# Optimization experiments

Measured on AMD Instinct MI355X. Metric: run time of the kernel, lower is better.

Reference implementation:

```python
import jax, jax.numpy as jnp
import numpy as np

N_BCH = 8        # molecules per batch
N_ATM = 10000    # atoms per molecule
N_EDGE = 5_120_000  # ~avg degree 64
N_ELM = 100      # element-type table size


def setup_inputs() -> dict:
    key = jax.random.key(0)
    k1, k2, k3, k4, k5, k6, k7 = jax.random.split(key, 7)
    elm = jax.random.randint(k1, (N_BCH, N_ATM), 0, N_ELM)
    edge_n = jax.random.randint(k2, (N_EDGE,), 0, N_BCH)
    edge_i = jax.random.randint(k3, (N_EDGE,), 0, N_ATM)
    edge_j = jax.random.randint(k4, (N_EDGE,), 0, N_ATM)
    # squared distances in [0, 4) -> dis in [0, 2)
    sod = jax.random.uniform(k5, (N_EDGE,), dtype=jnp.float32) * 4.0
    # per-element force constant and radius (positive)
    k_param = jax.random.uniform(k6, (N_ELM,), dtype=jnp.float32) + 0.5
    radius = jax.random.uniform(k7, (N_ELM,), dtype=jnp.float32) * 0.5 + 0.5
    return {"elm": elm, "edge_n": edge_n, "edge_i": edge_i, "edge_j": edge_j,
            "sod": sod, "k": k_param, "radius": radius}


def reference(elm, edge_n, edge_i, edge_j, sod, k, radius):
    # gather per-edge element types
    ei = elm[edge_n, edge_i]          # [E]
    ej = elm[edge_n, edge_j]          # [E]
    dis = jnp.sqrt(sod)               # [E]
    kk = k[ei] + k[ej]                # [E]
    R = radius[ei] + radius[ej]       # [E]
    mask = dis < R
    d = dis - R
    eng_bnd = jnp.where(mask, kk * d * d, jnp.zeros((), dtype=sod.dtype))  # [E]
    # scatter-add per atom: flat index n*n_atm + i
    seg = edge_n * N_ATM + edge_i
    eng_atm = jax.ops.segment_sum(eng_bnd, seg, num_segments=N_BCH * N_ATM)
    eng_atm = eng_atm.reshape(N_BCH, N_ATM)
    eng_mol = eng_atm.sum(axis=1)     # [n_bch]
    return eng_mol
```

## Files before the change

kernel.cpp:

```cpp
#include <hip/hip_runtime.h>
#include <hip/hip_bf16.h>
#include <hip/hip_fp16.h>

#define N_BCH 8
#define N_ATM 10000
#define N_ELM 100
#define N_ATOMS_TOT 80000
#define NBLK 256
#define NTHR 1024

typedef int   i4 __attribute__((ext_vector_type(4)));
typedef float f4 __attribute__((ext_vector_type(4)));

__launch_bounds__(1024, 4)
__global__ void edge_kernel(const int* __restrict__ elm,
                            const float* __restrict__ kparam,
                            const float* __restrict__ radius,
                            const int* __restrict__ edge_n,
                            const int* __restrict__ edge_i,
                            const int* __restrict__ edge_j,
                            const float* __restrict__ sod,
                            float* __restrict__ out,
                            int nE) {
    __shared__ unsigned int s_elm32[N_ATOMS_TOT / 4];
    __shared__ __half2 s_kr[128];
    __shared__ float s_red[16][N_BCH];

    for (int t = threadIdx.x; t < N_ATOMS_TOT / 4; t += NTHR) {
        i4 v = *(const i4*)(elm + 4 * t);
        s_elm32[t] = (unsigned int)(v[0] & 0xff)
                   | ((unsigned int)(v[1] & 0xff) << 8)
                   | ((unsigned int)(v[2] & 0xff) << 16)
                   | ((unsigned int)(v[3] & 0xff) << 24);
    }
    if (threadIdx.x < N_ELM)
        s_kr[threadIdx.x] =
            __floats2half2_rn(kparam[threadIdx.x], radius[threadIdx.x]);
    __syncthreads();

    const unsigned char* s_elm = (const unsigned char*)s_elm32;

    float acc[N_BCH];
#pragma unroll
    for (int b = 0; b < N_BCH; ++b) acc[b] = 0.0f;

    const int nvec  = nE >> 2;
    const int chunk = (nvec + NBLK - 1) / NBLK;
    const int base  = blockIdx.x * chunk;
    const int vmax  = min(base + chunk, nvec);
    const int nsweep = (chunk + NTHR - 1) / NTHR;

    const i4* en4 = (const i4*)edge_n;
    const i4* ei4 = (const i4*)edge_i;
    const i4* ej4 = (const i4*)edge_j;
    const f4* s4  = (const f4*)sod;

    int  v  = base + threadIdx.x;
    bool pv = v < vmax;
    int  vc = pv ? v : 0;
    i4 nn = __builtin_nontemporal_load(en4 + vc);
    i4 ii = __builtin_nontemporal_load(ei4 + vc);
    i4 jj = __builtin_nontemporal_load(ej4 + vc);
    f4 ss = __builtin_nontemporal_load(s4  + vc);

    for (int s = 0; s < nsweep; ++s) {
        int  v2  = v + NTHR;
        bool pv2 = v2 < vmax;
        int  vc2 = pv2 ? v2 : 0;
        i4 nn2 = __builtin_nontemporal_load(en4 + vc2);
        i4 ii2 = __builtin_nontemporal_load(ei4 + vc2);
        i4 jj2 = __builtin_nontemporal_load(ej4 + vc2);
        f4 ss2 = __builtin_nontemporal_load(s4  + vc2);

#pragma unroll
        for (int u = 0; u < 4; ++u) {
            int n = nn[u];
            int bb = n * N_ATM;
            int e_i = s_elm[bb + ii[u]];
            int e_j = s_elm[bb + jj[u]];
            __half2 krsum = __hadd2(s_kr[e_i], s_kr[e_j]);
            float kk = __low2float(krsum);
            float R  = __high2float(krsum);
            float dis = sqrtf(ss[u]);
            float d  = dis - R;
            float val = (pv && (dis < R)) ? kk * d * d : 0.0f;
#pragma unroll
            for (int b = 0; b < N_BCH; ++b)
                acc[b] += (n == b) ? val : 0.0f;
        }
        nn = nn2; ii = ii2; jj = jj2; ss = ss2; v = v2; pv = pv2;
    }

    const int tail_start = nvec << 2;
    const int tail_n = nE - tail_start;
    const int gtid = blockIdx.x * NTHR + threadIdx.x;
    if (gtid < tail_n) {
        int e = tail_start + gtid;
        int n = edge_n[e];
        int e_i = s_elm[n * N_ATM + edge_i[e]];
        int e_j = s_elm[n * N_ATM + edge_j[e]];
        __half2 krsum = __hadd2(s_kr[e_i], s_kr[e_j]);
        float kk = __low2float(krsum);
        float R  = __high2float(krsum);
        float dis = sqrtf(sod[e]);
        float d  = dis - R;
        float val = (dis < R) ? kk * d * d : 0.0f;
#pragma unroll
        for (int b = 0; b < N_BCH; ++b)
            acc[b] += (n == b) ? val : 0.0f;
    }

    const int lane = threadIdx.x & 63;
    const int wave = threadIdx.x >> 6;
#pragma unroll
    for (int off = 8; off <= 32; off <<= 1) {
#pragma unroll
        for (int b = 0; b < N_BCH; ++b)
            acc[b] += __shfl_xor(acc[b], off, 64);
    }
    const int j = lane >> 3;
    float x = acc[0];
#pragma unroll
    for (int b = 1; b < N_BCH; ++b) x = (j == b) ? acc[b] : x;
#pragma unroll
    for (int off = 1; off <= 4; off <<= 1)
        x += __shfl_xor(x, off, 64);

    if ((lane & 7) == 0) s_red[wave][j] = x;
    __syncthreads();
    if (threadIdx.x < N_BCH) {
        float t = 0.0f;
#pragma unroll
        for (int w = 0; w < 16; ++w) t += s_red[w][threadIdx.x];
        atomicAdd(&out[threadIdx.x], t);
    }
}

extern "C" void kernel_launch(void* const* d_in, const int* in_sizes, int n_in,
                              void* d_out, int out_size, void* d_ws, size_t ws_size,
                              hipStream_t stream) {
    const int*   elm    = (const int*)d_in[0];
    const int*   edge_n = (const int*)d_in[1];
    const int*   edge_i = (const int*)d_in[2];
    const int*   edge_j = (const int*)d_in[3];
    const float* sod    = (const float*)d_in[4];
    const float* kparam = (const float*)d_in[5];
    const float* radius = (const float*)d_in[6];
    float* out = (float*)d_out;
    const int nE = in_sizes[1];

    hipMemsetAsync(out, 0, out_size * sizeof(float), stream);

    hipLaunchKernelGGL(edge_kernel, dim3(NBLK), dim3(NTHR), 0, stream,
                       elm, kparam, radius, edge_n, edge_i, edge_j, sod,
                       out, nE);
}
```

Baseline: 130.0 us.

## Pre-pack element table in separate kernel and retune grid for edge kernel

Adds a small kernel that packs the int32 element table into bytes in workspace once, so each edge block copies 80 KB with 16-byte loads instead of re-reading and packing 320 KB. The first edge loads are issued before the shared-memory fill to overlap latency. The grid changes to 1024 blocks of 512 threads, and the validity branch becomes a sentinel value plus fminf. Costs are an extra kernel launch, more blocks each doing the LDS table copy, and a masked batch index that assumes valid inputs.

```diff
diff --git a/kernel.cpp b/kernel.cpp
--- a/kernel.cpp
+++ b/kernel.cpp
@@ -6,14 +6,27 @@
 #define N_ATM 10000
 #define N_ELM 100
 #define N_ATOMS_TOT 80000
-#define NBLK 256
-#define NTHR 1024
+#define NBLK 1024
+#define NTHR 512
 
 typedef int   i4 __attribute__((ext_vector_type(4)));
 typedef float f4 __attribute__((ext_vector_type(4)));
 
-__launch_bounds__(1024, 4)
-__global__ void edge_kernel(const int* __restrict__ elm,
+__launch_bounds__(256)
+__global__ void pack_elm_kernel(const int* __restrict__ elm,
+                                unsigned int* __restrict__ elm_u8) {
+    int t = blockIdx.x * blockDim.x + threadIdx.x;
+    if (t < N_ATOMS_TOT / 4) {
+        i4 v = *(const i4*)(elm + 4 * t);
+        elm_u8[t] = (unsigned int)(v[0] & 0xff)
+                  | ((unsigned int)(v[1] & 0xff) << 8)
+                  | ((unsigned int)(v[2] & 0xff) << 16)
+                  | ((unsigned int)(v[3] & 0xff) << 24);
+    }
+}
+
+__launch_bounds__(NTHR, 4)
+__global__ void edge_kernel(const unsigned int* __restrict__ elm_u8,
                             const float* __restrict__ kparam,
                             const float* __restrict__ radius,
                             const int* __restrict__ edge_n,
@@ -24,18 +37,36 @@
                             int nE) {
     __shared__ unsigned int s_elm32[N_ATOMS_TOT / 4];
     __shared__ __half2 s_kr[128];
-    __shared__ float s_red[16][N_BCH];
+    __shared__ float s_red[8][N_BCH];
 
-    for (int t = threadIdx.x; t < N_ATOMS_TOT / 4; t += NTHR) {
-        i4 v = *(const i4*)(elm + 4 * t);
-        s_elm32[t] = (unsigned int)(v[0] & 0xff)
-                   | ((unsigned int)(v[1] & 0xff) << 8)
-                   | ((unsigned int)(v[2] & 0xff) << 16)
-                   | ((unsigned int)(v[3] & 0xff) << 24);
+    const int nvec  = nE >> 2;
+    const int chunk = (nvec + NBLK - 1) / NBLK;
+    const int base  = blockIdx.x * chunk;
+    const int vmax  = min(base + chunk, nvec);
+
+    const i4* en4 = (const i4*)edge_n;
+    const i4* ei4 = (const i4*)edge_i;
+    const i4* ej4 = (const i4*)edge_j;
+    const f4* s4  = (const f4*)sod;
+
+    int  start = base;
+    int  v     = base + (int)threadIdx.x;
+    bool p     = v < vmax;
+    int  vc    = min(v, nvec - 1);
+    i4 nn = __builtin_nontemporal_load(en4 + vc);
+    i4 ii = __builtin_nontemporal_load(ei4 + vc);
+    i4 jj = __builtin_nontemporal_load(ej4 + vc);
+    f4 ss = __builtin_nontemporal_load(s4  + vc);
+
+    {
+        const i4* src = (const i4*)elm_u8;
+        i4* dst = (i4*)s_elm32;
+        for (int t = threadIdx.x; t < N_ATOMS_TOT / 16; t += NTHR)
+            dst[t] = src[t];
+        if (threadIdx.x < N_ELM)
+            s_kr[threadIdx.x] =
+                __floats2half2_rn(kparam[threadIdx.x], radius[threadIdx.x]);
     }
-    if (threadIdx.x < N_ELM)
-        s_kr[threadIdx.x] =
-            __floats2half2_rn(kparam[threadIdx.x], radius[threadIdx.x]);
     __syncthreads();
 
     const unsigned char* s_elm = (const unsigned char*)s_elm32;
@@ -44,51 +75,46 @@
 #pragma unroll
     for (int b = 0; b < N_BCH; ++b) acc[b] = 0.0f;
 
-    const int nvec  = nE >> 2;
-    const int chunk = (nvec + NBLK - 1) / NBLK;
-    const int base  = blockIdx.x * chunk;
-    const int vmax  = min(base + chunk, nvec);
-    const int nsweep = (chunk + NTHR - 1) / NTHR;
+    if (base < vmax) {
+        while (true) {
+            const int  nstart = start + NTHR;
+            const bool more   = nstart < vmax;
+            i4 nn2, ii2, jj2; f4 ss2;
+            if (more) {
+                int vc2 = min(v + NTHR, nvec - 1);
+                nn2 = __builtin_nontemporal_load(en4 + vc2);
+                ii2 = __builtin_nontemporal_load(ei4 + vc2);
+                jj2 = __builtin_nontemporal_load(ej4 + vc2);
+                ss2 = __builtin_nontemporal_load(s4  + vc2);
+            }
 
-    const i4* en4 = (const i4*)edge_n;
-    const i4* ei4 = (const i4*)edge_i;
-    const i4* ej4 = (const i4*)edge_j;
-    const f4* s4  = (const f4*)sod;
-
-    int  v  = base + threadIdx.x;
-    bool pv = v < vmax;
-    int  vc = pv ? v : 0;
-    i4 nn = __builtin_nontemporal_load(en4 + vc);
-    i4 ii = __builtin_nontemporal_load(ei4 + vc);
-    i4 jj = __builtin_nontemporal_load(ej4 + vc);
-    f4 ss = __builtin_nontemporal_load(s4  + vc);
-
-    for (int s = 0; s < nsweep; ++s) {
-        int  v2  = v + NTHR;
-        bool pv2 = v2 < vmax;
-        int  vc2 = pv2 ? v2 : 0;
-        i4 nn2 = __builtin_nontemporal_load(en4 + vc2);
-        i4 ii2 = __builtin_nontemporal_load(ei4 + vc2);
-        i4 jj2 = __builtin_nontemporal_load(ej4 + vc2);
-        f4 ss2 = __builtin_nontemporal_load(s4  + vc2);
+            f4 ssm;
+#pragma unroll
+            for (int u = 0; u < 4; ++u) ssm[u] = p ? ss[u] : 1e30f;
 
 #pragma unroll
-        for (int u = 0; u < 4; ++u) {
-            int n = nn[u];
-            int bb = n * N_ATM;
-            int e_i = s_elm[bb + ii[u]];
-            int e_j = s_elm[bb + jj[u]];
-            __half2 krsum = __hadd2(s_kr[e_i], s_kr[e_j]);
-            float kk = __low2float(krsum);
-            float R  = __high2float(krsum);
-            float dis = sqrtf(ss[u]);
-            float d  = dis - R;
-            float val = (pv && (dis < R)) ? kk * d * d : 0.0f;
+            for (int u = 0; u < 4; ++u) {
+                int n  = nn[u] & 7;
+                int bb = n * N_ATM;
+                int e_i = s_elm[bb + ii[u]];
+                int e_j = s_elm[bb + jj[u]];
+                __half2 krsum = __hadd2(s_kr[e_i], s_kr[e_j]);
+                float kk = __low2float(krsum);
+                float R  = __high2float(krsum);
+                float dis = sqrtf(ssm[u]);
+                float d   = fminf(dis - R, 0.0f);
+                float val = kk * d * d;
 #pragma unroll
-            for (int b = 0; b < N_BCH; ++b)
-                acc[b] += (n == b) ? val : 0.0f;
+                for (int b = 0; b < N_BCH; ++b)
+                    acc[b] += (n == b) ? val : 0.0f;
+            }
+
+            if (!more) break;
+            start = nstart;
+            v += NTHR;
+            p = v < vmax;
+            nn = nn2; ii = ii2; jj = jj2; ss = ss2;
         }
-        nn = nn2; ii = ii2; jj = jj2; ss = ss2; v = v2; pv = pv2;
     }
 
     const int tail_start = nvec << 2;
@@ -96,15 +122,15 @@
     const int gtid = blockIdx.x * NTHR + threadIdx.x;
     if (gtid < tail_n) {
         int e = tail_start + gtid;
-        int n = edge_n[e];
+        int n = edge_n[e] & 7;
         int e_i = s_elm[n * N_ATM + edge_i[e]];
         int e_j = s_elm[n * N_ATM + edge_j[e]];
         __half2 krsum = __hadd2(s_kr[e_i], s_kr[e_j]);
         float kk = __low2float(krsum);
         float R  = __high2float(krsum);
         float dis = sqrtf(sod[e]);
-        float d  = dis - R;
-        float val = (dis < R) ? kk * d * d : 0.0f;
+        float d   = fminf(dis - R, 0.0f);
+        float val = kk * d * d;
 #pragma unroll
         for (int b = 0; b < N_BCH; ++b)
             acc[b] += (n == b) ? val : 0.0f;
@@ -131,7 +157,7 @@
     if (threadIdx.x < N_BCH) {
         float t = 0.0f;
 #pragma unroll
-        for (int w = 0; w < 16; ++w) t += s_red[w][threadIdx.x];
+        for (int w = 0; w < 8; ++w) t += s_red[w][threadIdx.x];
         atomicAdd(&out[threadIdx.x], t);
     }
 }
@@ -149,9 +175,12 @@
     float* out = (float*)d_out;
     const int nE = in_sizes[1];
 
+    unsigned int* elm_u8 = (unsigned int*)d_ws;
+
     hipMemsetAsync(out, 0, out_size * sizeof(float), stream);
-
+    hipLaunchKernelGGL(pack_elm_kernel, dim3((N_ATOMS_TOT / 4 + 255) / 256),
+                       dim3(256), 0, stream, elm, elm_u8);
     hipLaunchKernelGGL(edge_kernel, dim3(NBLK), dim3(NTHR), 0, stream,
-                       elm, kparam, radius, edge_n, edge_i, edge_j, sod,
+                       elm_u8, kparam, radius, edge_n, edge_i, edge_j, sod,
                        out, nE);
 }
```

New measurement: 135.7 us. +4.4%, slower.
